# Performance work log

Hardware: AMD Instinct MI355X
Metric: run time of the kernel (lower is better)

Reference implementation:

```python
import jax, jax.numpy as jnp
import numpy as np

N_NODE, N_USER, N_PRICE, EMB = 100000, 40000, 100, 128
E_VV, E_VP, E_VU, E_UV = 2000000, 200000, 2000000, 2000000


def _spmm(rows, cols, vals, x, n_rows):
    # sparse COO (n_rows, n_cols) @ x  -> (n_rows, d)
    return jax.ops.segment_sum(vals[:, None] * x[cols], rows, num_segments=n_rows)


def _row_norm_spmm(rows, cols, vals, x, n_rows):
    # torch.sparse.mm followed by division by row-sum of values (+1e-8)
    num = _spmm(rows, cols, vals, x, n_rows)
    den = jax.ops.segment_sum(vals, rows, num_segments=n_rows)[:, None] + 1e-8
    return num / den


def _linear(x, W, b):
    return x @ W.T + b


def setup_inputs() -> dict:
    key = jax.random.key(0)
    ks = jax.random.split(key, 40)
    d = {}
    d['embedding'] = jax.random.normal(ks[0], (N_NODE, EMB), jnp.float32) * 0.1
    d['pri_emb'] = jax.random.normal(ks[1], (N_PRICE, EMB), jnp.float32) * 0.1
    d['user_emb'] = jax.random.normal(ks[2], (N_USER, EMB), jnp.float32) * 0.1
    d['adj_rows'] = jax.random.randint(ks[3], (E_VV,), 0, N_NODE, jnp.int32)
    d['adj_cols'] = jax.random.randint(ks[4], (E_VV,), 0, N_NODE, jnp.int32)
    d['adj_vals'] = jax.random.uniform(ks[5], (E_VV,), jnp.float32)
    d['vp_rows'] = jax.random.randint(ks[6], (E_VP,), 0, N_NODE, jnp.int32)
    d['vp_cols'] = jax.random.randint(ks[7], (E_VP,), 0, N_PRICE, jnp.int32)
    d['vp_vals'] = jax.random.uniform(ks[8], (E_VP,), jnp.float32)
    d['vu_rows'] = jax.random.randint(ks[9], (E_VU,), 0, N_NODE, jnp.int32)
    d['vu_cols'] = jax.random.randint(ks[10], (E_VU,), 0, N_USER, jnp.int32)
    d['vu_vals'] = jax.random.uniform(ks[11], (E_VU,), jnp.float32)
    d['pv_rows'] = jax.random.randint(ks[12], (E_VP,), 0, N_PRICE, jnp.int32)
    d['pv_cols'] = jax.random.randint(ks[13], (E_VP,), 0, N_NODE, jnp.int32)
    d['pv_vals'] = jax.random.uniform(ks[14], (E_VP,), jnp.float32)
    d['uv_rows'] = jax.random.randint(ks[15], (E_UV,), 0, N_USER, jnp.int32)
    d['uv_cols'] = jax.random.randint(ks[16], (E_UV,), 0, N_NODE, jnp.int32)
    d['uv_vals'] = jax.random.uniform(ks[17], (E_UV,), jnp.float32)
    d['item_price_indices'] = jax.random.randint(ks[18], (N_NODE,), 0, N_PRICE, jnp.int32)
    s = 0.02
    d['mat_vu'] = jax.random.normal(ks[19], (N_NODE, 1), jnp.float32) * s
    d['mat_pv'] = jax.random.normal(ks[20], (N_PRICE, 1), jnp.float32) * s
    d['mat_uv'] = jax.random.normal(ks[21], (N_USER, 1), jnp.float32) * s
    d['W_aogi'] = jax.random.normal(ks[22], (EMB, 2 * EMB), jnp.float32) * s
    d['b_aogi'] = jnp.zeros((EMB,), jnp.float32)
    d['W_bgi1'] = jax.random.normal(ks[23], (EMB, EMB), jnp.float32) * s
    d['b_bgi1'] = jnp.zeros((EMB,), jnp.float32)
    d['W_aogp'] = jax.random.normal(ks[24], (EMB, 2 * EMB), jnp.float32) * s
    d['b_aogp'] = jnp.zeros((EMB,), jnp.float32)
    d['W_bgp1'] = jax.random.normal(ks[25], (EMB, EMB), jnp.float32) * s
    d['b_bgp1'] = jnp.zeros((EMB,), jnp.float32)
    d['W_user'] = jax.random.normal(ks[26], (EMB, 3 * EMB), jnp.float32) * s
    d['b_user'] = jnp.zeros((EMB,), jnp.float32)
    d['user_lambda'] = jnp.asarray(0.2, jnp.float32)
    return d


def _forward(embedding, pri_emb, user_emb,
             adj_rows, adj_cols, adj_vals,
             vp_rows, vp_cols, vp_vals,
             vu_rows, vu_cols, vu_vals,
             pv_rows, pv_cols, pv_vals,
             uv_rows, uv_cols, uv_vals,
             item_price_indices,
             mat_vu, mat_pv, mat_uv,
             W_aogi, b_aogi, W_bgi1, b_bgi1,
             W_aogp, b_aogp, W_bgp1, b_bgp1,
             W_user, b_user, user_lambda,
             layers=1):
    def inter_gate(Wa, ba, Wb, bb, e1, e2):
        gate = jax.nn.sigmoid(_linear(jnp.concatenate([e1, e2], 1), Wa, ba) + _linear(e1, Wb, bb))
        return e1 + gate * e2  # dropout50 = identity at eval

    def intra_gate(rows, cols, vals, mat_v, emb2, n_rows):
        # torch version computes the chunked row-normalized spmm under no_grad
        alpha = jax.lax.stop_gradient(_row_norm_spmm(rows, cols, vals, emb2, n_rows))
        return alpha * mat_v  # dropout70 = identity at eval

    for _ in range(layers):
        item = (inter_gate(W_aogi, b_aogi, W_bgi1, b_bgi1, embedding,
                           _spmm(vp_rows, vp_cols, vp_vals, pri_emb, N_NODE))
                + _spmm(adj_rows, adj_cols, adj_vals, embedding, N_NODE)
                + user_lambda * intra_gate(vu_rows, vu_cols, vu_vals, mat_vu, user_emb, N_NODE))
        price = inter_gate(W_aogp, b_aogp, W_bgp1, b_bgp1, pri_emb,
                           intra_gate(pv_rows, pv_cols, pv_vals, mat_pv, embedding, N_PRICE))
        e_price_user = _spmm(uv_rows, uv_cols, uv_vals, pri_emb[item_price_indices], N_USER)
        e_item_user = intra_gate(uv_rows, uv_cols, uv_vals, mat_uv, embedding, N_USER)
        gate = jax.nn.sigmoid(_linear(jnp.concatenate([user_emb, e_item_user, e_price_user], -1), W_user, b_user))
        user = gate * user_emb + (1.0 - gate) * e_item_user
        embedding, pri_emb, user_emb = item, price, user
    return item, price, user


def reference(embedding, pri_emb, user_emb,
              adj_rows, adj_cols, adj_vals,
              vp_rows, vp_cols, vp_vals,
              vu_rows, vu_cols, vu_vals,
              pv_rows, pv_cols, pv_vals,
              uv_rows, uv_cols, uv_vals,
              item_price_indices,
              mat_vu, mat_pv, mat_uv,
              W_aogi, b_aogi, W_bgi1, b_bgi1,
              W_aogp, b_aogp, W_bgp1, b_bgp1,
              W_user, b_user, user_lambda):
    return _forward(embedding, pri_emb, user_emb,
                    adj_rows, adj_cols, adj_vals,
                    vp_rows, vp_cols, vp_vals,
                    vu_rows, vu_cols, vu_vals,
                    pv_rows, pv_cols, pv_vals,
                    uv_rows, uv_cols, uv_vals,
                    item_price_indices,
                    mat_vu, mat_pv, mat_uv,
                    W_aogi, b_aogi, W_bgi1, b_bgi1,
                    W_aogp, b_aogp, W_bgp1, b_bgp1,
                    W_user, b_user, user_lambda)
```

## Files before the change

kernel.cpp:

```cpp
#include <hip/hip_runtime.h>
#include <hip/hip_bf16.h>

#define N_NODE 100000
#define N_USER 40000
#define N_PRICE 100
#define EMB 128
#define E_VV 2000000
#define E_VP 200000
#define E_VU 2000000
#define E_UV 2000000

#define FOFF0 0
#define FOFF1 256
#define FOFF2 512
#define FOFF3 767
#define FOFF4 1023
#define FTOT  1073
#define EPB   8192
#define BK1 245
#define BK2 490
#define BK3 735
#define BK4 760
#define BKT 785
#define CB1 256
#define CB2 512
#define CB3 767
#define CB4 1023
#define CBT 1073
#define RB_PV   100
#define RB_ITEM 25000
#define RB_USER 10000
#define RBT (RB_PV + RB_ITEM + RB_USER)
#define FB_ITEM 782
#define FB_USER 313
#define FBT (FB_ITEM + FB_USER + 50)

typedef __attribute__((ext_vector_type(8))) short short8;
typedef __attribute__((ext_vector_type(4))) float f32x4;

__device__ __forceinline__ float sigf(float x){ return 1.f/(1.f+__expf(-x)); }
__device__ __forceinline__ unsigned bfr(float f){
  unsigned u = __float_as_uint(f);
  return (u + 0x7FFFu + ((u>>16)&1u)) >> 16;
}
__device__ __forceinline__ float bf_lo(unsigned u){ return __uint_as_float(u << 16); }
__device__ __forceinline__ float bf_hi(unsigned u){ return __uint_as_float(u & 0xFFFF0000u); }
__device__ __forceinline__ unsigned pack2(float x, float y){ return bfr(x) | (bfr(y)<<16); }

__global__ __launch_bounds__(256) void k_cvt_all(
    const float4* __restrict__ se, const float4* __restrict__ su, const float4* __restrict__ sp,
    uint2* __restrict__ de, uint2* __restrict__ du, uint2* __restrict__ dp){
  const int nE = N_NODE*EMB/4, nU = N_USER*EMB/4, nP = N_PRICE*EMB/4;
  int i = blockIdx.x*256 + threadIdx.x;
  const float4* src; uint2* dst; int j;
  if (i < nE){ src = se; dst = de; j = i; }
  else if (i < nE+nU){ src = su; dst = du; j = i-nE; }
  else if (i < nE+nU+nP){ src = sp; dst = dp; j = i-nE-nU; }
  else return;
  float4 v = src[j];
  dst[j] = make_uint2(bfr(v.x) | (bfr(v.y)<<16), bfr(v.z) | (bfr(v.w)<<16));
}

__global__ __launch_bounds__(256) void k_prep(
    const float* __restrict__ Wa, const float* __restrict__ Wb, const float* __restrict__ Wu,
    ushort* __restrict__ Wc, ushort* __restrict__ Wub,
    int* __restrict__ fill,
    int2* __restrict__ adjE, int2* __restrict__ vuE, int2* __restrict__ uvE,
    int2* __restrict__ vpE, int2* __restrict__ pvE){
  if (blockIdx.x == 320){
    int t = threadIdx.x;
    for (int i = t; i < FTOT; i += 256) fill[i] = 0;
    if (t < 16){
      int2 z = make_int2(0,0);
      adjE[E_VV+t] = z; vuE[E_VU+t] = z; uvE[E_UV+t] = z; vpE[E_VP+t] = z; pvE[E_VP+t] = z;
    }
    return;
  }
  int idx = blockIdx.x*256 + threadIdx.x;
  if (idx < 128*256){
    int n = idx >> 8, k = idx & 255;
    float v = Wa[n*256+k] + ((k < 128) ? Wb[n*128+k] : 0.f);
    Wc[idx] = (ushort)bfr(v);
  } else {
    int j = idx - 128*256;
    if (j < 128*384) Wub[j] = (ushort)bfr(Wu[j]);
  }
}

template<int E, int RPB, int NB, int CAPc>
__device__ __forceinline__ void bucket_body(int blk,
    const int* __restrict__ rows, const int* __restrict__ cols, const float* __restrict__ vals,
    int* __restrict__ fill, uint2* __restrict__ stg, int* cnt, int* gbase)
{
  const int t = threadIdx.x;
  const int e0 = blk * EPB;
  for (int i = t; i < NB; i += 256) cnt[i] = 0;
  __syncthreads();
  int rr[32];
  #pragma unroll
  for (int i = 0; i < 32; ++i){
    int e = e0 + i*256 + t;
    rr[i] = (e < E) ? rows[e] : -1;
    if (rr[i] >= 0) atomicAdd(&cnt[rr[i]/RPB], 1);
  }
  __syncthreads();
  for (int b = t; b < NB; b += 256){
    int c = cnt[b];
    gbase[b] = (c > 0) ? atomicAdd(&fill[b], c) : 0;
    cnt[b] = 0;
  }
  __syncthreads();
  #pragma unroll
  for (int i = 0; i < 32; ++i){
    if (rr[i] >= 0){
      int e = e0 + i*256 + t;
      int b = rr[i]/RPB, rl = rr[i] - b*RPB;
      int slot = gbase[b] + atomicAdd(&cnt[b], 1);
      if (slot >= CAPc) slot = CAPc - 1;
      stg[(size_t)b*CAPc + slot] = make_uint2((unsigned)cols[e] | ((unsigned)rl << 17), __float_as_uint(vals[e]));
    }
  }
}

__global__ __launch_bounds__(256) void k_bucket_all(
    const int* __restrict__ aR, const int* __restrict__ aC, const float* __restrict__ aV,
    const int* __restrict__ uR, const int* __restrict__ uC, const float* __restrict__ uV,
    const int* __restrict__ vR, const int* __restrict__ vC, const float* __restrict__ vV,
    const int* __restrict__ pR, const int* __restrict__ pC, const float* __restrict__ pV,
    const int* __restrict__ qR, const int* __restrict__ qC, const float* __restrict__ qV,
    int* __restrict__ fill,
    uint2* __restrict__ stgA, uint2* __restrict__ stgU, uint2* __restrict__ stgV,
    uint2* __restrict__ stgP, uint2* __restrict__ stgQ)
{
  __shared__ int cnt[256], gbase[256];
  int b = blockIdx.x;
  if      (b < BK1) bucket_body<E_VV,391,256,8704>(b,      aR,aC,aV, fill+FOFF0, stgA, cnt, gbase);
  else if (b < BK2) bucket_body<E_VU,391,256,8704>(b-BK1,  uR,uC,uV, fill+FOFF1, stgU, cnt, gbase);
  else if (b < BK3) bucket_body<E_UV,157,255,8704>(b-BK2,  vR,vC,vV, fill+FOFF2, stgV, cnt, gbase);
  else if (b < BK4) bucket_body<E_VP,391,256,1536>(b-BK3,  pR,pC,pV, fill+FOFF3, stgP, cnt, gbase);
  else              bucket_body<E_VP,  2, 50,5120>(b-BK4,  qR,qC,qV, fill+FOFF4, stgQ, cnt, gbase);
}

template<int NROW, int RPB, int NB, int CAPc>
__device__ __forceinline__ void csr_body(int b,
    const uint2* __restrict__ stg, const int* __restrict__ fill,
    int* __restrict__ start, int2* __restrict__ csr, int* cnt, int* sbase)
{
  const int t = threadIdx.x;
  const int row0 = b * RPB;
  int R = NROW - row0; if (R > RPB) R = RPB;
  int count = fill[b]; if (count > CAPc) count = CAPc;
  for (int i = t; i < R; i += 256) cnt[i] = 0;
  if (t < 64){
    int run = 0;
    for (int c0 = 0; c0 < NB; c0 += 64){
      int j = c0 + t;
      int x = (j < NB) ? fill[j] : 0;
      int s = x;
      #pragma unroll
      for (int d = 1; d < 64; d <<= 1){ int y = __shfl_up(s, d); if (t >= d) s += y; }
      if (j == b) *sbase = run + s - x;
      run += __shfl(s, 63);
    }
  }
  __syncthreads();
  const int base = *sbase;
  const uint2* mystg = stg + (size_t)b*CAPc;
  for (int j = t; j < count; j += 256)
    atomicAdd(&cnt[mystg[j].x >> 17], 1);
  __syncthreads();
  if (t < 64){
    int run = 0;
    for (int c0 = 0; c0 < R; c0 += 64){
      int i = c0 + t;
      int x = (i < R) ? cnt[i] : 0;
      int s = x;
      #pragma unroll
      for (int d = 1; d < 64; d <<= 1){ int y = __shfl_up(s, d); if (t >= d) s += y; }
      if (i < R) cnt[i] = run + s - x;
      run += __shfl(s, 63);
    }
  }
  __syncthreads();
  for (int i = t; i < R; i += 256) start[row0 + i] = base + cnt[i];
  if (b == NB-1 && t == 0) start[NROW] = base + count;
  __syncthreads();
  for (int j = t; j < count; j += 256){
    uint2 kv = mystg[j];
    int rl = kv.x >> 17;
    int pos = base + atomicAdd(&cnt[rl], 1);
    csr[pos] = make_int2((int)(kv.x & 0x1FFFF), (int)kv.y);
  }
}

__global__ __launch_bounds__(256) void k_csr_all(
    const uint2* __restrict__ stgA, const uint2* __restrict__ stgU, const uint2* __restrict__ stgV,
    const uint2* __restrict__ stgP, const uint2* __restrict__ stgQ,
    const int* __restrict__ fill,
    int* __restrict__ aS, int* __restrict__ uS, int* __restrict__ vS,
    int* __restrict__ pS, int* __restrict__ qS,
    int2* __restrict__ aE, int2* __restrict__ uE, int2* __restrict__ vE,
    int2* __restrict__ pE, int2* __restrict__ qE)
{
  __shared__ int cnt[391];
  __shared__ int sbase;
  int b = blockIdx.x;
  if      (b < CB1) csr_body<N_NODE,391,256,8704>(b,     stgA, fill+FOFF0, aS, aE, cnt, &sbase);
  else if (b < CB2) csr_body<N_NODE,391,256,8704>(b-CB1, stgU, fill+FOFF1, uS, uE, cnt, &sbase);
  else if (b < CB3) csr_body<N_USER,157,255,8704>(b-CB2, stgV, fill+FOFF2, vS, vE, cnt, &sbase);
  else if (b < CB4) csr_body<N_NODE,391,256,1536>(b-CB3, stgP, fill+FOFF3, pS, pE, cnt, &sbase);
  else              csr_body<N_PRICE,  2, 50,5120>(b-CB4, stgQ, fill+FOFF4, qS, qE, cnt, &sbase);
}


#define FMA8(ACC, U, V)                                     \
  ACC[0] += (V)*bf_lo((U).x); ACC[1] += (V)*bf_hi((U).x);   \
  ACC[2] += (V)*bf_lo((U).y); ACC[3] += (V)*bf_hi((U).y);   \
  ACC[4] += (V)*bf_lo((U).z); ACC[5] += (V)*bf_hi((U).z);   \
  ACC[6] += (V)*bf_lo((U).w); ACC[7] += (V)*bf_hi((U).w);

#define RED8(ACC)                                           \
  _Pragma("unroll")                                         \
  for (int j = 0; j < 8; ++j){                              \
    ACC[j] += __shfl_xor(ACC[j], 16);                       \
    ACC[j] += __shfl_xor(ACC[j], 32);                       \
  }

__device__ __forceinline__ void item_body(int rb,
    const uint4* __restrict__ be4, const uint4* __restrict__ bu4, const uint4* __restrict__ bp4,
    const int* __restrict__ aS, const int2* __restrict__ aE,
    const int* __restrict__ uS, const int2* __restrict__ uE,
    const int* __restrict__ pS, const int2* __restrict__ pE,
    const float* __restrict__ mat_vu, const float* __restrict__ lam,
    float4* __restrict__ out4, uint4* __restrict__ vp4)
{
  const int r = rb*4 + (threadIdx.x >> 6);
  const int l = threadIdx.x & 63;
  const int g = l >> 4, q = l & 15;
  float aA[8] = {}, aU[8] = {}, aP[8] = {};
  float den = 0.f;
  int s = aS[r], e = aS[r+1];
  for (int i = s; i < e; i += 16){
    int2 cv[4]; uint4 u[4];
    #pragma unroll
    for (int k = 0; k < 4; ++k) cv[k] = aE[i + 4*k + g];
    #pragma unroll
    for (int k = 0; k < 4; ++k) u[k] = be4[(size_t)cv[k].x*16 + q];
    #pragma unroll
    for (int k = 0; k < 4; ++k){
      float v = (i + 4*k + g < e) ? __int_as_float(cv[k].y) : 0.f;
      FMA8(aA, u[k], v)
    }
  }
  s = uS[r]; e = uS[r+1];
  for (int i = s; i < e; i += 16){
    int2 cv[4]; uint4 u[4];
    #pragma unroll
    for (int k = 0; k < 4; ++k) cv[k] = uE[i + 4*k + g];
    #pragma unroll
    for (int k = 0; k < 4; ++k) u[k] = bu4[(size_t)cv[k].x*16 + q];
    #pragma unroll
    for (int k = 0; k < 4; ++k){
      float v = (i + 4*k + g < e) ? __int_as_float(cv[k].y) : 0.f;
      FMA8(aU, u[k], v)
      den += v;
    }
  }
  s = pS[r]; e = pS[r+1];
  for (int i = s; i < e; i += 16){
    int2 cv[4]; uint4 u[4];
    #pragma unroll
    for (int k = 0; k < 4; ++k) cv[k] = pE[i + 4*k + g];
    #pragma unroll
    for (int k = 0; k < 4; ++k) u[k] = bp4[(size_t)cv[k].x*16 + q];
    #pragma unroll
    for (int k = 0; k < 4; ++k){
      float v = (i + 4*k + g < e) ? __int_as_float(cv[k].y) : 0.f;
      FMA8(aP, u[k], v)
    }
  }
  RED8(aA) RED8(aU) RED8(aP)
  den += __shfl_xor(den, 16); den += __shfl_xor(den, 32);
  float sc = lam[0]*mat_vu[r]/(den + 1e-8f);
  if (g == 0){
    out4[(size_t)r*32 + q*2]     = make_float4(aA[0]+sc*aU[0], aA[1]+sc*aU[1], aA[2]+sc*aU[2], aA[3]+sc*aU[3]);
    out4[(size_t)r*32 + q*2 + 1] = make_float4(aA[4]+sc*aU[4], aA[5]+sc*aU[5], aA[6]+sc*aU[6], aA[7]+sc*aU[7]);
    vp4[(size_t)r*16 + q] = make_uint4(pack2(aP[0],aP[1]), pack2(aP[2],aP[3]), pack2(aP[4],aP[5]), pack2(aP[6],aP[7]));
  }
}

__device__ __forceinline__ void user_body(int rb,
    const uint4* __restrict__ be4, const uint4* __restrict__ bp4,
    const int* __restrict__ S, const int2* __restrict__ E,
    const int* __restrict__ ipi, const float* __restrict__ mat_uv,
    uint4* __restrict__ eit4, uint4* __restrict__ uvp4)
{
  const int r = rb*4 + (threadIdx.x >> 6);
  const int l = threadIdx.x & 63;
  const int g = l >> 4, q = l & 15;
  float aI[8] = {}, aP[8] = {};
  float den = 0.f;
  int s = S[r], e = S[r+1];
  for (int i = s; i < e; i += 8){
    int2 cv[2];
    #pragma unroll
    for (int k = 0; k < 2; ++k) cv[k] = E[i + 4*k + g];
    uint4 u[2]; int ip[2];
    #pragma unroll
    for (int k = 0; k < 2; ++k){ u[k] = be4[(size_t)cv[k].x*16 + q]; ip[k] = ipi[cv[k].x]; }
    uint4 y[2];
    #pragma unroll
    for (int k = 0; k < 2; ++k) y[k] = bp4[(size_t)ip[k]*16 + q];
    #pragma unroll
    for (int k = 0; k < 2; ++k){
      float v = (i + 4*k + g < e) ? __int_as_float(cv[k].y) : 0.f;
      FMA8(aI, u[k], v)
      FMA8(aP, y[k], v)
      den += v;
    }
  }
  RED8(aI) RED8(aP)
  den += __shfl_xor(den, 16); den += __shfl_xor(den, 32);
  float sc = mat_uv[r]/(den + 1e-8f);
  if (g == 0){
    eit4[(size_t)r*16 + q] = make_uint4(pack2(sc*aI[0],sc*aI[1]), pack2(sc*aI[2],sc*aI[3]),
                                        pack2(sc*aI[4],sc*aI[5]), pack2(sc*aI[6],sc*aI[7]));
    uvp4[(size_t)r*16 + q] = make_uint4(pack2(aP[0],aP[1]), pack2(aP[2],aP[3]),
                                        pack2(aP[4],aP[5]), pack2(aP[6],aP[7]));
  }
}

__device__ __forceinline__ void pv_body(int r,
    const uint4* __restrict__ be4, const int2* __restrict__ E, const int* __restrict__ S,
    float* __restrict__ num, float* __restrict__ den_out)
{
  const int t = threadIdx.x;
  const int wid = t >> 6, l = t & 63;
  const int g = l >> 4, q = l & 15;
  float aP[8] = {}; float den = 0.f;
  int s = S[r], e = S[r+1];
  for (int i0 = s + wid*16; i0 < e; i0 += 64){
    int2 cv[4]; uint4 u[4];
    #pragma unroll
    for (int k = 0; k < 4; ++k) cv[k] = E[i0 + 4*k + g];
    #pragma unroll
    for (int k = 0; k < 4; ++k) u[k] = be4[(size_t)cv[k].x*16 + q];
    #pragma unroll
    for (int k = 0; k < 4; ++k){
      float v = (i0 + 4*k + g < e) ? __int_as_float(cv[k].y) : 0.f;
      FMA8(aP, u[k], v)
      den += v;
    }
  }
  RED8(aP)
  den += __shfl_xor(den, 16); den += __shfl_xor(den, 32);
  __shared__ float red[4][16][8];
  __shared__ float dred[4];
  if (g == 0){
    #pragma unroll
    for (int j = 0; j < 8; ++j) red[wid][q][j] = aP[j];
    if (l == 0) dred[wid] = den;
  }
  __syncthreads();
  if (t < 16){
    #pragma unroll
    for (int j = 0; j < 8; ++j)
      num[r*128 + t*8 + j] = red[0][t][j] + red[1][t][j] + red[2][t][j] + red[3][t][j];
    if (t == 0) den_out[r] = dred[0] + dred[1] + dred[2] + dred[3];
  }
}

__global__ __launch_bounds__(256) void k_rows_all(
    const uint4* __restrict__ be4, const uint4* __restrict__ bu4, const uint4* __restrict__ bp4,
    const int* __restrict__ aS, const int2* __restrict__ aE,
    const int* __restrict__ uS, const int2* __restrict__ uE,
    const int* __restrict__ pS, const int2* __restrict__ pE,
    const int* __restrict__ vS, const int2* __restrict__ vE,
    const int* __restrict__ qS, const int2* __restrict__ qE,
    const int* __restrict__ ipi,
    const float* __restrict__ mat_vu, const float* __restrict__ mat_uv, const float* __restrict__ lam,
    float4* __restrict__ out4, uint4* __restrict__ vp4,
    uint4* __restrict__ eit4, uint4* __restrict__ uvp4,
    float* __restrict__ pv_num, float* __restrict__ pv_den)
{
  int b = blockIdx.x;
  if (b < RB_PV){ pv_body(b, be4, qE, qS, pv_num, pv_den); return; }
  b -= RB_PV;
  if (b < RB_ITEM){ item_body(b, be4, bu4, bp4, aS, aE, uS, uE, pS, pE, mat_vu, lam, out4, vp4); return; }
  b -= RB_ITEM;
  user_body(b, be4, bp4, vS, vE, ipi, mat_uv, eit4, uvp4);
}

__device__ __forceinline__ void item_final_body(int blk, ushort* As, ushort* Bs,
    const ushort* __restrict__ A0, const ushort* __restrict__ A1,
    const ushort* __restrict__ W,
    const float* __restrict__ ba, const float* __restrict__ bb,
    const float* __restrict__ emb, float* __restrict__ out)
{
  const int t = threadIdx.x;
  const int l = t & 63, wv = t >> 6;
  const int wr = (wv>>1)*64, wc = (wv&1)*64;
  const int row0 = blk*128;
  const int lr16 = t >> 3;
  const int slot = t & 7;
  f32x4 acc[4][4] = {};
  for (int s = 0; s < 4; ++s){
    if (s) __syncthreads();
    const int k0 = s*64;
    const ushort* srcA = (k0 < 128) ? (A0 + k0) : (A1 + (k0 - 128));
    #pragma unroll
    for (int i = 0; i < 4; ++i){
      int r = i*32 + lr16;
      int gr = row0 + r; if (gr >= N_NODE) gr = N_NODE-1;
      uint4 va = *(const uint4*)(srcA + (size_t)gr*128 + slot*8);
      *(uint4*)&As[r*64 + ((slot*8) ^ ((r&7)*8))] = va;
      uint4 vb = *(const uint4*)(W + r*256 + k0 + slot*8);
      *(uint4*)&Bs[r*64 + ((slot*8) ^ ((r&7)*8))] = vb;
    }
    __syncthreads();
    #pragma unroll
    for (int kk = 0; kk < 64; kk += 32){
      short8 af[4], bf[4];
      #pragma unroll
      for (int f = 0; f < 4; ++f){
        int ar = wr + f*16 + (l&15);
        af[f] = *(const short8*)&As[ar*64 + ((kk + (l>>4)*8) ^ ((ar&7)*8))];
        int bn = wc + f*16 + (l&15);
        bf[f] = *(const short8*)&Bs[bn*64 + ((kk + (l>>4)*8) ^ ((bn&7)*8))];
      }
      #pragma unroll
      for (int fi = 0; fi < 4; ++fi)
        #pragma unroll
        for (int fj = 0; fj < 4; ++fj)
          acc[fi][fj] = __builtin_amdgcn_mfma_f32_16x16x32_bf16(af[fi], bf[fj], acc[fi][fj], 0, 0, 0);
    }
  }
  const int g4 = (l>>4)*4;
  #pragma unroll
  for (int fi = 0; fi < 4; ++fi){
    #pragma unroll
    for (int r = 0; r < 4; ++r){
      int grow = row0 + wr + fi*16 + g4 + r;
      if (grow < N_NODE){
        #pragma unroll
        for (int fj = 0; fj < 4; ++fj){
          int col = wc + fj*16 + (l&15);
          float x = acc[fi][fj][r] + ba[col] + bb[col];
          unsigned pv2 = *(const unsigned*)&A1[(size_t)grow*128 + (col & ~1)];
          float v = (col & 1) ? bf_hi(pv2) : bf_lo(pv2);
          size_t o = (size_t)grow*128 + col;
          out[o] = emb[o] + sigf(x)*v + out[o];
        }
      }
    }
  }
}

__device__ __forceinline__ void user_final_body(int blk, ushort* As, ushort* Bs,
    const ushort* __restrict__ A0, const ushort* __restrict__ A1, const ushort* __restrict__ A2,
    const ushort* __restrict__ W,
    const float* __restrict__ bu,
    const float* __restrict__ ue, float* __restrict__ out)
{
  const int t = threadIdx.x;
  const int l = t & 63, wv = t >> 6;
  const int wr = (wv>>1)*64, wc = (wv&1)*64;
  const int row0 = blk*128;
  const int lr16 = t >> 3;
  const int slot = t & 7;
  f32x4 acc[4][4] = {};
  for (int s = 0; s < 6; ++s){
    if (s) __syncthreads();
    const int k0 = s*64;
    const ushort* base = (s < 2) ? A0 : ((s < 4) ? A1 : A2);
    const ushort* srcA = base + (s & 1)*64;
    #pragma unroll
    for (int i = 0; i < 4; ++i){
      int r = i*32 + lr16;
      int gr = row0 + r; if (gr >= N_USER) gr = N_USER-1;
      uint4 va = *(const uint4*)(srcA + (size_t)gr*128 + slot*8);
      *(uint4*)&As[r*64 + ((slot*8) ^ ((r&7)*8))] = va;
      uint4 vb = *(const uint4*)(W + r*384 + k0 + slot*8);
      *(uint4*)&Bs[r*64 + ((slot*8) ^ ((r&7)*8))] = vb;
    }
    __syncthreads();
    #pragma unroll
    for (int kk = 0; kk < 64; kk += 32){
      short8 af[4], bf[4];
      #pragma unroll
      for (int f = 0; f < 4; ++f){
        int ar = wr + f*16 + (l&15);
        af[f] = *(const short8*)&As[ar*64 + ((kk + (l>>4)*8) ^ ((ar&7)*8))];
        int bn = wc + f*16 + (l&15);
        bf[f] = *(const short8*)&Bs[bn*64 + ((kk + (l>>4)*8) ^ ((bn&7)*8))];
      }
      #pragma unroll
      for (int fi = 0; fi < 4; ++fi)
        #pragma unroll
        for (int fj = 0; fj < 4; ++fj)
          acc[fi][fj] = __builtin_amdgcn_mfma_f32_16x16x32_bf16(af[fi], bf[fj], acc[fi][fj], 0, 0, 0);
    }
  }
  const int g4 = (l>>4)*4;
  #pragma unroll
  for (int fi = 0; fi < 4; ++fi){
    #pragma unroll
    for (int r = 0; r < 4; ++r){
      int grow = row0 + wr + fi*16 + g4 + r;
      if (grow < N_USER){
        #pragma unroll
        for (int fj = 0; fj < 4; ++fj){
          int col = wc + fj*16 + (l&15);
          float g = sigf(acc[fi][fj][r] + bu[col]);
          unsigned e2 = *(const unsigned*)&A1[(size_t)grow*128 + (col & ~1)];
          float ei = (col & 1) ? bf_hi(e2) : bf_lo(e2);
          size_t o = (size_t)grow*128 + col;
          out[o] = g*ue[o] + (1.f - g)*ei;
        }
      }
    }
  }
}

__device__ __forceinline__ void price_final_body(int blk, float* A2,
    const float* __restrict__ pe, const float* __restrict__ num, const float* __restrict__ den,
    const float* __restrict__ mat_pv,
    const float* __restrict__ Wa, const float* __restrict__ ba,
    const float* __restrict__ Wb, const float* __restrict__ bb,
    float* __restrict__ out_price)
{
  int t = threadIdx.x;
  #pragma unroll
  for (int i = 0; i < 2; ++i){
    int flat = i*256 + t;
    int rl = flat >> 8; int k = flat & 255;
    int r = blk*2 + rl;
    float v;
    if (k < 128) v = pe[r*128 + k];
    else         v = num[r*128 + (k-128)] / (den[r] + 1e-8f) * mat_pv[r];
    A2[rl*256 + k] = v;
  }
  __syncthreads();
  int rl = t >> 7; int c = t & 127;
  int r = blk*2 + rl;
  float x = 0.f;
  #pragma unroll 4
  for (int k = 0; k < 256; ++k){
    float w = (k < 128) ? (Wa[c*256 + k] + Wb[c*128 + k]) : Wa[c*256 + k];
    x += A2[rl*256 + k]*w;
  }
  float g = sigf(x + ba[c] + bb[c]);
  out_price[r*128 + c] = pe[r*128 + c] + g*A2[rl*256 + 128 + c];
}

__global__ __launch_bounds__(256) void k_finals_all(
    const ushort* __restrict__ bemb, const ushort* __restrict__ vp_bf, const ushort* __restrict__ Wc,
    const float* __restrict__ b_aogi, const float* __restrict__ b_bgi1,
    const float* __restrict__ emb, float* __restrict__ out_item,
    const ushort* __restrict__ bue, const ushort* __restrict__ eitem_bf, const ushort* __restrict__ uvp_bf,
    const ushort* __restrict__ Wub, const float* __restrict__ b_user,
    const float* __restrict__ ue, float* __restrict__ out_user,
    const float* __restrict__ pe, const float* __restrict__ pv_num, const float* __restrict__ pv_den,
    const float* __restrict__ mat_pv,
    const float* __restrict__ W_aogp, const float* __restrict__ b_aogp,
    const float* __restrict__ W_bgp1, const float* __restrict__ b_bgp1,
    float* __restrict__ out_price)
{
  __shared__ __align__(16) ushort As[128*64];
  __shared__ __align__(16) ushort Bs[128*64];
  __shared__ float A2[512];
  int b = blockIdx.x;
  if (b < FB_ITEM){
    item_final_body(b, As, Bs, bemb, vp_bf, Wc, b_aogi, b_bgi1, emb, out_item);
  } else if (b < FB_ITEM + FB_USER){
    user_final_body(b - FB_ITEM, As, Bs, bue, eitem_bf, uvp_bf, Wub, b_user, ue, out_user);
  } else {
    price_final_body(b - FB_ITEM - FB_USER, A2, pe, pv_num, pv_den, mat_pv,
                     W_aogp, b_aogp, W_bgp1, b_bgp1, out_price);
  }
}

extern "C" void kernel_launch(void* const* d_in, const int* in_sizes, int n_in,
                              void* d_out, int out_size, void* d_ws, size_t ws_size,
                              hipStream_t stream){
  (void)in_sizes; (void)n_in; (void)out_size; (void)ws_size;
  const float* emb = (const float*)d_in[0];
  const float* pe  = (const float*)d_in[1];
  const float* ue  = (const float*)d_in[2];
  const int*   adj_r = (const int*)d_in[3];  const int* adj_c = (const int*)d_in[4];  const float* adj_v = (const float*)d_in[5];
  const int*   vp_r  = (const int*)d_in[6];  const int* vp_c  = (const int*)d_in[7];  const float* vp_v  = (const float*)d_in[8];
  const int*   vu_r  = (const int*)d_in[9];  const int* vu_c  = (const int*)d_in[10]; const float* vu_v  = (const float*)d_in[11];
  const int*   pv_r  = (const int*)d_in[12]; const int* pv_c  = (const int*)d_in[13]; const float* pv_v  = (const float*)d_in[14];
  const int*   uv_r  = (const int*)d_in[15]; const int* uv_c  = (const int*)d_in[16]; const float* uv_v  = (const float*)d_in[17];
  const int*   ipi   = (const int*)d_in[18];
  const float* mat_vu = (const float*)d_in[19];
  const float* mat_pv = (const float*)d_in[20];
  const float* mat_uv = (const float*)d_in[21];
  const float* W_aogi = (const float*)d_in[22]; const float* b_aogi = (const float*)d_in[23];
  const float* W_bgi1 = (const float*)d_in[24]; const float* b_bgi1 = (const float*)d_in[25];
  const float* W_aogp = (const float*)d_in[26]; const float* b_aogp = (const float*)d_in[27];
  const float* W_bgp1 = (const float*)d_in[28]; const float* b_bgp1 = (const float*)d_in[29];
  const float* W_user = (const float*)d_in[30]; const float* b_user = (const float*)d_in[31];
  const float* lam    = (const float*)d_in[32];

  float* out_item  = (float*)d_out;
  float* out_price = out_item + (size_t)N_NODE*EMB;
  float* out_user  = out_price + (size_t)N_PRICE*EMB;

  char* w = (char*)d_ws;
  size_t off = 0;
  auto alloc = [&](size_t bytes)->char*{
    char* p = w + off;
    off = (off + bytes + 255) & ~(size_t)255;
    return p;
  };
  int* fill = (int*)alloc(FTOT*4);
  int* aS  = (int*)alloc((N_NODE+1)*4);
  int* uS  = (int*)alloc((N_NODE+1)*4);
  int* vS  = (int*)alloc((N_USER+1)*4);
  int* pS  = (int*)alloc((N_NODE+1)*4);
  int* qS  = (int*)alloc(101*4);
  ushort* Wc_item = (ushort*)alloc(128*256*2);
  ushort* Wu_bf   = (ushort*)alloc(128*384*2);
  char* region = alloc((size_t)93*1024*1024);
  uint2* stgA = (uint2*)region;
  uint2* stgU = (uint2*)(region + (size_t)256*8704*8);
  uint2* stgV = (uint2*)(region + (size_t)2*256*8704*8);
  uint2* stgP = (uint2*)(region + (size_t)3*256*8704*8);
  uint2* stgQ = (uint2*)(region + (size_t)3*256*8704*8 + (size_t)256*1536*8);
  unsigned* bemb = (unsigned*)region;
  unsigned* bue  = (unsigned*)(region + (size_t)N_NODE*EMB*2);
  unsigned* bpe  = (unsigned*)(region + (size_t)(N_NODE+N_USER)*EMB*2);
  unsigned* vp_bf = (unsigned*)(region + (size_t)37*1024*1024);
  int2*  adjE = (int2*)alloc(((size_t)E_VV+16)*8);
  int2*  vuE  = (int2*)alloc(((size_t)E_VU+16)*8);
  int2*  uvE  = (int2*)alloc(((size_t)E_UV+16)*8);
  int2*  vpE  = (int2*)alloc(((size_t)E_VP+16)*8);
  int2*  pvE  = (int2*)alloc(((size_t)E_VP+16)*8);
  unsigned* eitem_bf = (unsigned*)alloc((size_t)N_USER*64*4);
  unsigned* uvp_bf   = (unsigned*)alloc((size_t)N_USER*64*4);
  float* pv_num   = (float*)alloc((size_t)N_PRICE*EMB*4);
  float* pv_den   = (float*)alloc(N_PRICE*4);

  k_prep<<<321,256,0,stream>>>(W_aogi, W_bgi1, W_user, Wc_item, Wu_bf,
                               fill, adjE, vuE, uvE, vpE, pvE);

  k_bucket_all<<<BKT,256,0,stream>>>(
      adj_r,adj_c,adj_v, vu_r,vu_c,vu_v, uv_r,uv_c,uv_v, vp_r,vp_c,vp_v, pv_r,pv_c,pv_v,
      fill, stgA, stgU, stgV, stgP, stgQ);

  k_csr_all<<<CBT,256,0,stream>>>(stgA, stgU, stgV, stgP, stgQ, fill,
      aS, uS, vS, pS, qS, adjE, vuE, uvE, vpE, pvE);

  k_cvt_all<<<((N_NODE+N_USER+N_PRICE)*EMB/4+255)/256,256,0,stream>>>(
      (const float4*)emb, (const float4*)ue, (const float4*)pe,
      (uint2*)bemb, (uint2*)bue, (uint2*)bpe);

  k_rows_all<<<RBT,256,0,stream>>>(
      (const uint4*)bemb, (const uint4*)bue, (const uint4*)bpe,
      aS, adjE, uS, vuE, pS, vpE, vS, uvE, qS, pvE,
      ipi, mat_vu, mat_uv, lam,
      (float4*)out_item, (uint4*)vp_bf, (uint4*)eitem_bf, (uint4*)uvp_bf,
      pv_num, pv_den);

  k_finals_all<<<FBT,256,0,stream>>>(
      (const ushort*)bemb, (const ushort*)vp_bf, Wc_item, b_aogi, b_bgi1, emb, out_item,
      (const ushort*)bue, (const ushort*)eitem_bf, (const ushort*)uvp_bf, Wu_bf, b_user, ue, out_user,
      pe, pv_num, pv_den, mat_pv, W_aogp, b_aogp, W_bgp1, b_bgp1, out_price);
}
```

Measured before the change: 603.2 us.

## Stage bucket and CSR scatters in LDS and sort rows by column

The bucketing kernel now computes a local prefix over bucket counts and scatters edges into a shared-memory staging buffer. Each bucket is then written to global memory contiguously by one wavefront, replacing scattered per-edge global writes with coalesced ones. The CSR kernel likewise scatters into LDS, insertion-sorts each short row by its packed column key (which also orders deterministically), and writes the output sequentially. The intent is coalesced stores and better gather locality in later SpMM passes. The cost is large LDS use (64KB+), which reduces occupancy, plus serial per-thread sorting work.

After: 885.3 us. 46.8% more time.

```diff
diff --git a/kernel.cpp b/kernel.cpp
--- a/kernel.cpp
+++ b/kernel.cpp
@@ -90,34 +90,57 @@
 template<int E, int RPB, int NB, int CAPc>
 __device__ __forceinline__ void bucket_body(int blk,
     const int* __restrict__ rows, const int* __restrict__ cols, const float* __restrict__ vals,
-    int* __restrict__ fill, uint2* __restrict__ stg, int* cnt, int* gbase)
+    int* __restrict__ fill, uint2* __restrict__ stg,
+    int* cnt, int* gbase, int* lbase, uint2* stage)
 {
   const int t = threadIdx.x;
   const int e0 = blk * EPB;
   for (int i = t; i < NB; i += 256) cnt[i] = 0;
   __syncthreads();
-  int rr[32];
-  #pragma unroll
+  #pragma unroll 4
   for (int i = 0; i < 32; ++i){
     int e = e0 + i*256 + t;
-    rr[i] = (e < E) ? rows[e] : -1;
-    if (rr[i] >= 0) atomicAdd(&cnt[rr[i]/RPB], 1);
+    if (e < E) atomicAdd(&cnt[rows[e]/RPB], 1);
+  }
+  __syncthreads();
+  if (t < 64){
+    int run = 0;
+    for (int c0 = 0; c0 < NB; c0 += 64){
+      int j = c0 + t;
+      int x = (j < NB) ? cnt[j] : 0;
+      int s = x;
+      #pragma unroll
+      for (int d = 1; d < 64; d <<= 1){ int y = __shfl_up(s, d); if (t >= d) s += y; }
+      if (j < NB) lbase[j] = run + s - x;
+      run += __shfl(s, 63);
+    }
   }
   __syncthreads();
   for (int b = t; b < NB; b += 256){
     int c = cnt[b];
     gbase[b] = (c > 0) ? atomicAdd(&fill[b], c) : 0;
-    cnt[b] = 0;
-  }
-  __syncthreads();
-  #pragma unroll
+    cnt[b] = lbase[b];
+  }
+  __syncthreads();
+  #pragma unroll 4
   for (int i = 0; i < 32; ++i){
-    if (rr[i] >= 0){
-      int e = e0 + i*256 + t;
-      int b = rr[i]/RPB, rl = rr[i] - b*RPB;
-      int slot = gbase[b] + atomicAdd(&cnt[b], 1);
-      if (slot >= CAPc) slot = CAPc - 1;
-      stg[(size_t)b*CAPc + slot] = make_uint2((unsigned)cols[e] | ((unsigned)rl << 17), __float_as_uint(vals[e]));
+    int e = e0 + i*256 + t;
+    if (e < E){
+      int r = rows[e];
+      int b = r/RPB, rl = r - b*RPB;
+      int pos = atomicAdd(&cnt[b], 1);
+      stage[pos] = make_uint2((unsigned)cols[e] | ((unsigned)rl << 17), __float_as_uint(vals[e]));
+    }
+  }
+  __syncthreads();
+  const int wid = t >> 6, lane = t & 63;
+  for (int b = wid; b < NB; b += 4){
+    int lb = lbase[b];
+    int n = cnt[b] - lb;
+    int gb = gbase[b];
+    for (int j = lane; j < n; j += 64){
+      int slot = gb + j; if (slot >= CAPc) slot = CAPc - 1;
+      stg[(size_t)b*CAPc + slot] = stage[lb + j];
     }
   }
 }
@@ -132,19 +155,21 @@
     uint2* __restrict__ stgA, uint2* __restrict__ stgU, uint2* __restrict__ stgV,
     uint2* __restrict__ stgP, uint2* __restrict__ stgQ)
 {
-  __shared__ int cnt[256], gbase[256];
+  __shared__ int cnt[256], gbase[256], lbase[256];
+  __shared__ uint2 stage[EPB];
   int b = blockIdx.x;
-  if      (b < BK1) bucket_body<E_VV,391,256,8704>(b,      aR,aC,aV, fill+FOFF0, stgA, cnt, gbase);
-  else if (b < BK2) bucket_body<E_VU,391,256,8704>(b-BK1,  uR,uC,uV, fill+FOFF1, stgU, cnt, gbase);
-  else if (b < BK3) bucket_body<E_UV,157,255,8704>(b-BK2,  vR,vC,vV, fill+FOFF2, stgV, cnt, gbase);
-  else if (b < BK4) bucket_body<E_VP,391,256,1536>(b-BK3,  pR,pC,pV, fill+FOFF3, stgP, cnt, gbase);
-  else              bucket_body<E_VP,  2, 50,5120>(b-BK4,  qR,qC,qV, fill+FOFF4, stgQ, cnt, gbase);
+  if      (b < BK1) bucket_body<E_VV,391,256,8704>(b,      aR,aC,aV, fill+FOFF0, stgA, cnt, gbase, lbase, stage);
+  else if (b < BK2) bucket_body<E_VU,391,256,8704>(b-BK1,  uR,uC,uV, fill+FOFF1, stgU, cnt, gbase, lbase, stage);
+  else if (b < BK3) bucket_body<E_UV,157,255,8704>(b-BK2,  vR,vC,vV, fill+FOFF2, stgV, cnt, gbase, lbase, stage);
+  else if (b < BK4) bucket_body<E_VP,391,256,1536>(b-BK3,  pR,pC,pV, fill+FOFF3, stgP, cnt, gbase, lbase, stage);
+  else              bucket_body<E_VP,  2, 50,5120>(b-BK4,  qR,qC,qV, fill+FOFF4, stgQ, cnt, gbase, lbase, stage);
 }
 
 template<int NROW, int RPB, int NB, int CAPc>
 __device__ __forceinline__ void csr_body(int b,
     const uint2* __restrict__ stg, const int* __restrict__ fill,
-    int* __restrict__ start, int2* __restrict__ csr, int* cnt, int* sbase)
+    int* __restrict__ start, int2* __restrict__ csr,
+    int* cnt, int* rend, uint2* stage, int* sbase)
 {
   const int t = threadIdx.x;
   const int row0 = b * RPB;
@@ -182,14 +207,34 @@
     }
   }
   __syncthreads();
-  for (int i = t; i < R; i += 256) start[row0 + i] = base + cnt[i];
+  for (int i = t; i < R; i += 256){
+    rend[i] = cnt[i];
+    start[row0 + i] = base + cnt[i];
+  }
   if (b == NB-1 && t == 0) start[NROW] = base + count;
   __syncthreads();
   for (int j = t; j < count; j += 256){
     uint2 kv = mystg[j];
     int rl = kv.x >> 17;
-    int pos = base + atomicAdd(&cnt[rl], 1);
-    csr[pos] = make_int2((int)(kv.x & 0x1FFFF), (int)kv.y);
+    int pos = atomicAdd(&cnt[rl], 1);
+    stage[pos] = kv;
+  }
+  __syncthreads();
+  for (int i = t; i < R; i += 256){
+    int lo = rend[i], hi = cnt[i];
+    if (hi - lo > 1 && hi - lo <= 96){
+      for (int m = lo + 1; m < hi; ++m){
+        uint2 key = stage[m];
+        int j2 = m - 1;
+        while (j2 >= lo && stage[j2].x > key.x){ stage[j2+1] = stage[j2]; --j2; }
+        stage[j2+1] = key;
+      }
+    }
+  }
+  __syncthreads();
+  for (int j = t; j < count; j += 256){
+    uint2 kv = stage[j];
+    csr[base + j] = make_int2((int)(kv.x & 0x1FFFF), (int)kv.y);
   }
 }
 
@@ -202,14 +247,15 @@
     int2* __restrict__ aE, int2* __restrict__ uE, int2* __restrict__ vE,
     int2* __restrict__ pE, int2* __restrict__ qE)
 {
-  __shared__ int cnt[391];
+  __shared__ int cnt[391], rend[391];
   __shared__ int sbase;
+  __shared__ uint2 stage[8704];
   int b = blockIdx.x;
-  if      (b < CB1) csr_body<N_NODE,391,256,8704>(b,     stgA, fill+FOFF0, aS, aE, cnt, &sbase);
-  else if (b < CB2) csr_body<N_NODE,391,256,8704>(b-CB1, stgU, fill+FOFF1, uS, uE, cnt, &sbase);
-  else if (b < CB3) csr_body<N_USER,157,255,8704>(b-CB2, stgV, fill+FOFF2, vS, vE, cnt, &sbase);
-  else if (b < CB4) csr_body<N_NODE,391,256,1536>(b-CB3, stgP, fill+FOFF3, pS, pE, cnt, &sbase);
-  else              csr_body<N_PRICE,  2, 50,5120>(b-CB4, stgQ, fill+FOFF4, qS, qE, cnt, &sbase);
+  if      (b < CB1) csr_body<N_NODE,391,256,8704>(b,     stgA, fill+FOFF0, aS, aE, cnt, rend, stage, &sbase);
+  else if (b < CB2) csr_body<N_NODE,391,256,8704>(b-CB1, stgU, fill+FOFF1, uS, uE, cnt, rend, stage, &sbase);
+  else if (b < CB3) csr_body<N_USER,157,255,8704>(b-CB2, stgV, fill+FOFF2, vS, vE, cnt, rend, stage, &sbase);
+  else if (b < CB4) csr_body<N_NODE,391,256,1536>(b-CB3, stgP, fill+FOFF3, pS, pE, cnt, rend, stage, &sbase);
+  else              csr_body<N_PRICE,  2, 50,5120>(b-CB4, stgQ, fill+FOFF4, qS, qE, cnt, rend, stage, &sbase);
 }
 
 
```
